# Optimization experiments

Measured on AMD Instinct MI355X. Metric: run time of the kernel, lower is better.

## Reference

```python
import jax, jax.numpy as jnp
import numpy as np

N = 100000   # num_nodes
E = 1600000  # num_edges
H = 128      # hidden_dim
OUT = 1      # output_dim
SLOPE = 0.2  # GATConv leaky_relu negative_slope


def setup_inputs() -> dict:
    key = jax.random.key(0)
    ks = jax.random.split(key, 10)
    s = 1.0 / np.sqrt(H)
    return {
        "h": jnp.arange(N, dtype=jnp.int64 if jax.config.jax_enable_x64 else jnp.int32),
        "edge_index": jax.random.randint(ks[0], (2, E), 0, N),
        "node_type": jax.random.randint(ks[1], (N,), 0, 3),
        "emb": jax.random.normal(ks[2], (N, H), jnp.float32) * s,
        "W1": jax.random.normal(ks[3], (H, H), jnp.float32) * s,
        "a_src1": jax.random.normal(ks[4], (H,), jnp.float32) * s,
        "a_dst1": jax.random.normal(ks[5], (H,), jnp.float32) * s,
        "b1": jnp.zeros((H,), jnp.float32),
        "W2": jax.random.normal(ks[6], (H, OUT), jnp.float32) * s,
        "a_src2": jax.random.normal(ks[7], (OUT,), jnp.float32) * s,
        "a_dst2": jax.random.normal(ks[8], (OUT,), jnp.float32) * s,
        "b2": jnp.zeros((OUT,), jnp.float32),
    }


def gat_layer(x, src, dst, emask, W, a_src, a_dst, b, n_nodes):
    """PyG GATConv (heads=1, add_self_loops=True). Masked edges get -inf logits."""
    xp = x @ W                                  # [N, F]
    e_src = xp @ a_src                          # [N]
    e_dst = xp @ a_dst                          # [N]
    logits = jax.nn.leaky_relu(e_src[src] + e_dst[dst], SLOPE)   # [E]
    logits = jnp.where(emask, logits, -jnp.inf)
    self_logits = jax.nn.leaky_relu(e_src + e_dst, SLOPE)        # [N] self-loops
    # segment softmax over destination nodes (edges + self loop)
    m = jax.ops.segment_max(logits, dst, num_segments=n_nodes)
    m = jnp.maximum(m, self_logits)             # finite: self loop always present
    ew = jnp.exp(logits - m[dst])               # masked edges -> exp(-inf)=0
    sw = jnp.exp(self_logits - m)
    denom = jax.ops.segment_sum(ew, dst, num_segments=n_nodes) + sw
    alpha = ew / denom[dst]                     # [E]
    alpha_self = sw / denom                     # [N]
    out = jax.ops.segment_sum(alpha[:, None] * xp[src], dst, num_segments=n_nodes)
    out = out + alpha_self[:, None] * xp + b
    return out


def reference(h, edge_index, node_type, emb, W1, a_src1, a_dst1, b1, W2, a_src2, a_dst2, b2):
    src, dst = edge_index[0], edge_index[1]
    emask = (node_type[src] == 0) & (node_type[dst] == 0)
    x = emb[h]                                          # embedding lookup [N, H]
    x = gat_layer(x, src, dst, emask, W1, a_src1, a_dst1, b1, emb.shape[0])
    x = jax.nn.relu(x)
    x = gat_layer(x, src, dst, emask, W2, a_src2, a_dst2, b2, emb.shape[0])
    return x
```

## Files before the change

kernel.cpp:

```cpp
#include <hip/hip_runtime.h>

#define N_NODES 100000
#define N_EDGES 1600000
#define HD 128
#define SLOPE 0.2f
#define NBLK 391
#define GB 782
#define EB2 3125
#define CAP 32

typedef __attribute__((ext_vector_type(8))) short bf16x8;
typedef __attribute__((ext_vector_type(4))) float f32x4;

__device__ __forceinline__ unsigned short f2bf(float f) {
    union { float f; unsigned u; } v; v.f = f;
    const unsigned u = v.u + 0x7FFFu + ((v.u >> 16) & 1u);
    return (unsigned short)(u >> 16);
}
__device__ __forceinline__ unsigned pack2(float lo, float hi) {
    return (unsigned)f2bf(lo) | ((unsigned)f2bf(hi) << 16);
}
__device__ __forceinline__ float bf2f(unsigned u16) {
    union { unsigned u; float f; } v; v.u = u16 << 16; return v.f;
}

__global__ __launch_bounds__(256) void k0_zero(
    const int* __restrict__ nt, const float* __restrict__ W1,
    int* __restrict__ deg, unsigned* __restrict__ umask,
    unsigned short* __restrict__ W1bfT)
{
    const int i = blockIdx.x * 256 + threadIdx.x;
    bool act = false;
    if (i < N_NODES) { deg[i] = 0; act = (nt[i] == 0); }
    const unsigned long long bal = __ballot(act);
    const int lane = threadIdx.x & 63;
    if (lane == 0)       umask[i >> 5] = (unsigned)bal;
    else if (lane == 32) umask[i >> 5] = (unsigned)(bal >> 32);
    if (i < HD * HD) {
        const int n = i >> 7, k = i & 127;
        W1bfT[n * HD + k] = f2bf(W1[k * HD + n]);
    }
}

__global__ __launch_bounds__(512, 8) void k1_gemm_edge(
    const int* __restrict__ h,
    const float* __restrict__ emb,
    const unsigned short* __restrict__ W1bfT,
    const float* __restrict__ a_src1,
    const float* __restrict__ a_dst1,
    unsigned short* __restrict__ xp1,
    float* __restrict__ es1,
    float* __restrict__ ed1,
    float* __restrict__ denom1,
    const int* __restrict__ ei,
    const unsigned* __restrict__ umask,
    int* __restrict__ deg,
    int* __restrict__ adj)
{
    __shared__ unsigned short Wlds[HD * HD];
    const int tid = threadIdx.x;

    if (blockIdx.x >= GB) {
        const int e = (blockIdx.x - GB) * 512 + tid;
        const int src = ei[e];
        const int dst = ei[N_EDGES + e];
        const bool active =
            (((umask[src >> 5] >> (src & 31)) & (umask[dst >> 5] >> (dst & 31))) & 1u) != 0u;
        if (active) {
            const int slot = atomicAdd(deg + dst, 1);
            if (slot < CAP) adj[(size_t)dst * CAP + slot] = src;
        }
        return;
    }

    {
        const int n  = tid >> 2;
        const int kq = (tid & 3) * 32;
        const unsigned short* src = W1bfT + n * HD + kq;
        #pragma unroll
        for (int j = 0; j < 4; ++j) {
            const int c = (kq >> 3) + j;
            const int p = c ^ (n & 7);
            *(bf16x8*)(Wlds + n * HD + p * 8) = *(const bf16x8*)(src + j * 8);
        }
    }

    const int w   = tid >> 6;
    const int L   = tid & 63;
    const int lm  = L & 15;
    const int lg  = L >> 4;
    const int wrow0 = blockIdx.x * 128 + w * 16;

    const int arow = wrow0 + lm;
    const int g = (arow < N_NODES) ? arow : (N_NODES - 1);
    const float* xrow = emb + (size_t)h[g] * HD;

    __syncthreads();

    f32x4 acc[8];
    #pragma unroll
    for (int ct = 0; ct < 8; ++ct) acc[ct] = (f32x4)0.f;

    #pragma unroll
    for (int ks = 0; ks < 4; ++ks) {
        const int k0 = ks * 32 + lg * 8;
        const float4 u = *(const float4*)(xrow + k0);
        const float4 v = *(const float4*)(xrow + k0 + 4);
        union { bf16x8 b; unsigned x[4]; } t;
        t.x[0] = pack2(u.x, u.y);
        t.x[1] = pack2(u.z, u.w);
        t.x[2] = pack2(v.x, v.y);
        t.x[3] = pack2(v.z, v.w);
        const bf16x8 af = t.b;

        const int c = k0 >> 3;
        const int p = (c ^ (lm & 7)) * 8;
        #pragma unroll
        for (int ct = 0; ct < 8; ++ct) {
            const bf16x8 bfr = *(const bf16x8*)(Wlds + (ct * 16 + lm) * HD + p);
            acc[ct] = __builtin_amdgcn_mfma_f32_16x16x32_bf16(af, bfr, acc[ct], 0, 0, 0);
        }
    }

    float asv[8], adv[8];
    #pragma unroll
    for (int ct = 0; ct < 8; ++ct) {
        asv[ct] = a_src1[ct * 16 + lm];
        adv[ct] = a_dst1[ct * 16 + lm];
    }

    #pragma unroll
    for (int reg = 0; reg < 4; ++reg) {
        const int row = wrow0 + lg * 4 + reg;
        float s = 0.f, d = 0.f;
        #pragma unroll
        for (int ct = 0; ct < 8; ++ct) {
            s += acc[ct][reg] * asv[ct];
            d += acc[ct][reg] * adv[ct];
        }
        #pragma unroll
        for (int m = 1; m < 16; m <<= 1) {
            s += __shfl_xor(s, m, 64);
            d += __shfl_xor(d, m, 64);
        }
        if (row < N_NODES) {
            unsigned short* dst = xp1 + (size_t)row * HD;
            #pragma unroll
            for (int ct = 0; ct < 8; ++ct)
                dst[ct * 16 + lm] = f2bf(acc[ct][reg]);
            if (lm == 0) {
                const float sum = s + d;
                const float l = sum > 0.f ? sum : SLOPE * sum;
                es1[row] = s;
                ed1[row] = d;
                denom1[row] = __expf(l);
            }
        }
    }
}

__global__ __launch_bounds__(256) void k2_gather(
    const unsigned short* __restrict__ xp1, const float* __restrict__ denom1,
    const float* __restrict__ es1, const float* __restrict__ ed1,
    const int* __restrict__ deg, const int* __restrict__ adj,
    const float* __restrict__ b1, const float* __restrict__ W2,
    float* __restrict__ xp2)
{
    const int wid = threadIdx.x >> 6;
    const int lane = threadIdx.x & 63;
    const int i = blockIdx.x * 4 + wid;
    if (i >= N_NODES) return;

    const int dcount = min(deg[i], CAP);
    const float wself = denom1[i];
    const float edv   = ed1[i];
    const int* arow = adj + (size_t)i * CAP;

    const unsigned pself = ((const unsigned*)(xp1 + (size_t)i * HD))[lane];
    float a0 = wself * bf2f(pself & 0xFFFFu);
    float a1 = wself * bf2f(pself >> 16);
    float denom = wself;

    int sN = 0;
    if (dcount > 0) sN = arow[0];
    for (int j = 0; j < dcount; ++j) {
        const int s = sN;
        if (j + 1 < dcount) sN = arow[j + 1];
        const float lg = es1[s] + edv;
        const float l = lg > 0.f ? lg : SLOPE * lg;
        const float w = __expf(l);
        const unsigned pv = ((const unsigned*)(xp1 + (size_t)s * HD))[lane];
        a0 += w * bf2f(pv & 0xFFFFu);
        a1 += w * bf2f(pv >> 16);
        denom += w;
    }

    const float inv = 1.f / denom;
    const float o0 = fmaxf(a0 * inv + b1[2 * lane],     0.f);
    const float o1 = fmaxf(a1 * inv + b1[2 * lane + 1], 0.f);

    float part = o0 * W2[2 * lane] + o1 * W2[2 * lane + 1];
    #pragma unroll
    for (int off = 32; off > 0; off >>= 1) part += __shfl_down(part, off, 64);
    if (lane == 0) xp2[i] = part;
}

__global__ __launch_bounds__(256) void k3_final(
    const float* __restrict__ xp2, const int* __restrict__ deg,
    const int* __restrict__ adj,
    const float* __restrict__ a_src2, const float* __restrict__ a_dst2,
    const float* __restrict__ b2, float* __restrict__ out)
{
    const int i = blockIdx.x * 256 + threadIdx.x;
    if (i >= N_NODES) return;

    const float as = a_src2[0], ad = a_dst2[0];
    const float xi = xp2[i];
    const float s0 = (as + ad) * xi;
    const float l0 = s0 > 0.f ? s0 : SLOPE * s0;
    const float wself = __expf(l0);

    float denom = wself, num = wself * xi;
    const int dcount = min(deg[i], CAP);
    const int* arow = adj + (size_t)i * CAP;
    for (int j = 0; j < dcount; ++j) {
        const float xsv = xp2[arow[j]];
        const float lg = as * xsv + ad * xi;
        const float ll = lg > 0.f ? lg : SLOPE * lg;
        const float w = __expf(ll);
        denom += w;
        num += w * xsv;
    }
    out[i] = num / denom + b2[0];
}

extern "C" void kernel_launch(void* const* d_in, const int* in_sizes, int n_in,
                              void* d_out, int out_size, void* d_ws, size_t ws_size,
                              hipStream_t stream)
{
    const int* h   = (const int*)d_in[0];
    const int* ei  = (const int*)d_in[1];
    const int* nt  = (const int*)d_in[2];
    const float* emb    = (const float*)d_in[3];
    const float* W1     = (const float*)d_in[4];
    const float* a_src1 = (const float*)d_in[5];
    const float* a_dst1 = (const float*)d_in[6];
    const float* b1     = (const float*)d_in[7];
    const float* W2     = (const float*)d_in[8];
    const float* a_src2 = (const float*)d_in[9];
    const float* a_dst2 = (const float*)d_in[10];
    const float* b2     = (const float*)d_in[11];
    float* out = (float*)d_out;

    char* ws = (char*)d_ws;
    size_t off = 0;
    unsigned short* xp1 = (unsigned short*)(ws + off); off += (size_t)N_NODES * HD * sizeof(unsigned short);
    float* es1    = (float*)(ws + off); off += (size_t)N_NODES * sizeof(float);
    float* ed1    = (float*)(ws + off); off += (size_t)N_NODES * sizeof(float);
    float* denom1 = (float*)(ws + off); off += (size_t)N_NODES * sizeof(float);
    float* xp2    = (float*)(ws + off); off += (size_t)N_NODES * sizeof(float);
    int*   deg    = (int*)(ws + off);   off += (size_t)N_NODES * sizeof(int);
    unsigned* umask = (unsigned*)(ws + off); off += 3200 * sizeof(unsigned);
    unsigned short* W1bfT = (unsigned short*)(ws + off); off += (size_t)HD * HD * sizeof(unsigned short);
    off = (off + 255) & ~(size_t)255;
    int*   adj    = (int*)(ws + off);   off += (size_t)N_NODES * CAP * sizeof(int);

    k0_zero<<<NBLK, 256, 0, stream>>>(nt, W1, deg, umask, W1bfT);
    k1_gemm_edge<<<GB + EB2, 512, 0, stream>>>(
        h, emb, W1bfT, a_src1, a_dst1, xp1, es1, ed1, denom1,
        ei, umask, deg, adj);
    k2_gather<<<(N_NODES + 3) / 4, 256, 0, stream>>>(
        xp1, denom1, es1, ed1, deg, adj, b1, W2, xp2);
    k3_final<<<NBLK, 256, 0, stream>>>(
        xp2, deg, adj, a_src2, a_dst2, b2, out);
}
```

Measured before the change: 181.0 us.

## Persist GEMM/edge blocks, stage xp1 stores via LDS, precompute gather weights per lane

The fused GEMM/edge-binning kernel becomes a persistent grid of PB blocks that loop over the virtual block range. Its bf16 output tile is staged through shared memory so each row goes out as coalesced 16-byte stores instead of scattered 2-byte stores. The layer-1 gather now loads neighbour indices and computes attention weights once per lane, reduces the denominator with shuffles, then broadcasts index and weight while unrolling the feature accumulation by two. The layer-2 loop is also unrolled by two with paired index loads. The trade-offs are an extra LDS round trip plus barriers per tile, and a possible load-balance shift from the persistent loop.

Measured after the change: 218.0 us. 20.4% more time.

```diff
diff --git a/kernel.cpp b/kernel.cpp
--- a/kernel.cpp
+++ b/kernel.cpp
@@ -7,6 +7,7 @@
 #define NBLK 391
 #define GB 782
 #define EB2 3125
+#define PB 1024
 #define CAP 32
 
 typedef __attribute__((ext_vector_type(8))) short bf16x8;
@@ -60,100 +61,113 @@
     __shared__ unsigned short Wlds[HD * HD];
     const int tid = threadIdx.x;
 
-    if (blockIdx.x >= GB) {
-        const int e = (blockIdx.x - GB) * 512 + tid;
-        const int src = ei[e];
-        const int dst = ei[N_EDGES + e];
-        const bool active =
-            (((umask[src >> 5] >> (src & 31)) & (umask[dst >> 5] >> (dst & 31))) & 1u) != 0u;
-        if (active) {
-            const int slot = atomicAdd(deg + dst, 1);
-            if (slot < CAP) adj[(size_t)dst * CAP + slot] = src;
-        }
-        return;
-    }
-
-    {
-        const int n  = tid >> 2;
-        const int kq = (tid & 3) * 32;
-        const unsigned short* src = W1bfT + n * HD + kq;
-        #pragma unroll
-        for (int j = 0; j < 4; ++j) {
-            const int c = (kq >> 3) + j;
-            const int p = c ^ (n & 7);
-            *(bf16x8*)(Wlds + n * HD + p * 8) = *(const bf16x8*)(src + j * 8);
-        }
-    }
-
-    const int w   = tid >> 6;
-    const int L   = tid & 63;
-    const int lm  = L & 15;
-    const int lg  = L >> 4;
-    const int wrow0 = blockIdx.x * 128 + w * 16;
-
-    const int arow = wrow0 + lm;
-    const int g = (arow < N_NODES) ? arow : (N_NODES - 1);
-    const float* xrow = emb + (size_t)h[g] * HD;
-
-    __syncthreads();
-
-    f32x4 acc[8];
-    #pragma unroll
-    for (int ct = 0; ct < 8; ++ct) acc[ct] = (f32x4)0.f;
-
-    #pragma unroll
-    for (int ks = 0; ks < 4; ++ks) {
-        const int k0 = ks * 32 + lg * 8;
-        const float4 u = *(const float4*)(xrow + k0);
-        const float4 v = *(const float4*)(xrow + k0 + 4);
-        union { bf16x8 b; unsigned x[4]; } t;
-        t.x[0] = pack2(u.x, u.y);
-        t.x[1] = pack2(u.z, u.w);
-        t.x[2] = pack2(v.x, v.y);
-        t.x[3] = pack2(v.z, v.w);
-        const bf16x8 af = t.b;
-
-        const int c = k0 >> 3;
-        const int p = (c ^ (lm & 7)) * 8;
+    for (int vb = blockIdx.x; vb < GB + EB2; vb += PB) {
+        if (vb >= GB) {
+            const int e = (vb - GB) * 512 + tid;
+            const int src = ei[e];
+            const int dst = ei[N_EDGES + e];
+            const bool active =
+                (((umask[src >> 5] >> (src & 31)) & (umask[dst >> 5] >> (dst & 31))) & 1u) != 0u;
+            if (active) {
+                const int slot = atomicAdd(deg + dst, 1);
+                if (slot < CAP) adj[(size_t)dst * CAP + slot] = src;
+            }
+            continue;
+        }
+
+        {
+            const int n  = tid >> 2;
+            const int kq = (tid & 3) * 32;
+            const unsigned short* src = W1bfT + n * HD + kq;
+            #pragma unroll
+            for (int j = 0; j < 4; ++j) {
+                const int c = (kq >> 3) + j;
+                const int p = c ^ (n & 7);
+                *(bf16x8*)(Wlds + n * HD + p * 8) = *(const bf16x8*)(src + j * 8);
+            }
+        }
+
+        const int w   = tid >> 6;
+        const int L   = tid & 63;
+        const int lm  = L & 15;
+        const int lg  = L >> 4;
+        const int wrow0 = vb * 128 + w * 16;
+
+        const int arow = wrow0 + lm;
+        const int g = (arow < N_NODES) ? arow : (N_NODES - 1);
+        const float* xrow = emb + (size_t)h[g] * HD;
+
+        __syncthreads();
+
+        f32x4 acc[8];
+        #pragma unroll
+        for (int ct = 0; ct < 8; ++ct) acc[ct] = (f32x4)0.f;
+
+        #pragma unroll
+        for (int ks = 0; ks < 4; ++ks) {
+            const int k0 = ks * 32 + lg * 8;
+            const float4 u = *(const float4*)(xrow + k0);
+            const float4 v = *(const float4*)(xrow + k0 + 4);
+            union { bf16x8 b; unsigned x[4]; } t;
+            t.x[0] = pack2(u.x, u.y);
+            t.x[1] = pack2(u.z, u.w);
+            t.x[2] = pack2(v.x, v.y);
+            t.x[3] = pack2(v.z, v.w);
+            const bf16x8 af = t.b;
+
+            const int c = k0 >> 3;
+            const int p = (c ^ (lm & 7)) * 8;
+            #pragma unroll
+            for (int ct = 0; ct < 8; ++ct) {
+                const bf16x8 bfr = *(const bf16x8*)(Wlds + (ct * 16 + lm) * HD + p);
+                acc[ct] = __builtin_amdgcn_mfma_f32_16x16x32_bf16(af, bfr, acc[ct], 0, 0, 0);
+            }
+        }
+
+        float asv[8], adv[8];
         #pragma unroll
         for (int ct = 0; ct < 8; ++ct) {
-            const bf16x8 bfr = *(const bf16x8*)(Wlds + (ct * 16 + lm) * HD + p);
-            acc[ct] = __builtin_amdgcn_mfma_f32_16x16x32_bf16(af, bfr, acc[ct], 0, 0, 0);
-        }
-    }
-
-    float asv[8], adv[8];
-    #pragma unroll
-    for (int ct = 0; ct < 8; ++ct) {
-        asv[ct] = a_src1[ct * 16 + lm];
-        adv[ct] = a_dst1[ct * 16 + lm];
-    }
-
-    #pragma unroll
-    for (int reg = 0; reg < 4; ++reg) {
-        const int row = wrow0 + lg * 4 + reg;
-        float s = 0.f, d = 0.f;
-        #pragma unroll
-        for (int ct = 0; ct < 8; ++ct) {
-            s += acc[ct][reg] * asv[ct];
-            d += acc[ct][reg] * adv[ct];
-        }
-        #pragma unroll
-        for (int m = 1; m < 16; m <<= 1) {
-            s += __shfl_xor(s, m, 64);
-            d += __shfl_xor(d, m, 64);
-        }
-        if (row < N_NODES) {
-            unsigned short* dst = xp1 + (size_t)row * HD;
-            #pragma unroll
-            for (int ct = 0; ct < 8; ++ct)
-                dst[ct * 16 + lm] = f2bf(acc[ct][reg]);
-            if (lm == 0) {
+            asv[ct] = a_src1[ct * 16 + lm];
+            adv[ct] = a_dst1[ct * 16 + lm];
+        }
+
+        #pragma unroll
+        for (int reg = 0; reg < 4; ++reg) {
+            const int row = wrow0 + lg * 4 + reg;
+            float s = 0.f, d = 0.f;
+            #pragma unroll
+            for (int ct = 0; ct < 8; ++ct) {
+                s += acc[ct][reg] * asv[ct];
+                d += acc[ct][reg] * adv[ct];
+            }
+            #pragma unroll
+            for (int m = 1; m < 16; m <<= 1) {
+                s += __shfl_xor(s, m, 64);
+                d += __shfl_xor(d, m, 64);
+            }
+            if (row < N_NODES && lm == 0) {
                 const float sum = s + d;
                 const float l = sum > 0.f ? sum : SLOPE * sum;
                 es1[row] = s;
                 ed1[row] = d;
                 denom1[row] = __expf(l);
+            }
+        }
+
+        __syncthreads();
+        unsigned short* slice = Wlds + w * 2048;
+        #pragma unroll
+        for (int ct = 0; ct < 8; ++ct)
+            #pragma unroll
+            for (int reg = 0; reg < 4; ++reg)
+                slice[(lg * 4 + reg) * HD + ct * 16 + lm] = f2bf(acc[ct][reg]);
+        #pragma unroll
+        for (int rr = 0; rr < 4; ++rr) {
+            const int rl = rr * 4 + lg;
+            const int row = wrow0 + rl;
+            if (row < N_NODES) {
+                const bf16x8 vdat = *(const bf16x8*)(slice + rl * HD + lm * 8);
+                *(bf16x8*)(xp1 + (size_t)row * HD + lm * 8) = vdat;
             }
         }
     }
@@ -176,26 +190,40 @@
     const float edv   = ed1[i];
     const int* arow = adj + (size_t)i * CAP;
 
+    int nidx = 0; float nw = 0.f;
+    if (lane < dcount) {
+        nidx = arow[lane];
+        const float lgt = es1[nidx] + edv;
+        nw = __expf(lgt > 0.f ? lgt : SLOPE * lgt);
+    }
+    float dsum = nw;
+    #pragma unroll
+    for (int m = 32; m > 0; m >>= 1) dsum += __shfl_xor(dsum, m, 64);
+    const float inv = 1.f / (wself + dsum);
+
     const unsigned pself = ((const unsigned*)(xp1 + (size_t)i * HD))[lane];
     float a0 = wself * bf2f(pself & 0xFFFFu);
     float a1 = wself * bf2f(pself >> 16);
-    float denom = wself;
-
-    int sN = 0;
-    if (dcount > 0) sN = arow[0];
-    for (int j = 0; j < dcount; ++j) {
-        const int s = sN;
-        if (j + 1 < dcount) sN = arow[j + 1];
-        const float lg = es1[s] + edv;
-        const float l = lg > 0.f ? lg : SLOPE * lg;
-        const float w = __expf(l);
-        const unsigned pv = ((const unsigned*)(xp1 + (size_t)s * HD))[lane];
-        a0 += w * bf2f(pv & 0xFFFFu);
-        a1 += w * bf2f(pv >> 16);
-        denom += w;
-    }
-
-    const float inv = 1.f / denom;
+
+    int j = 0;
+    for (; j + 2 <= dcount; j += 2) {
+        const int   s0 = __shfl(nidx, j, 64);
+        const int   s1 = __shfl(nidx, j + 1, 64);
+        const float w0 = __shfl(nw, j, 64);
+        const float w1 = __shfl(nw, j + 1, 64);
+        const unsigned p0 = ((const unsigned*)(xp1 + (size_t)s0 * HD))[lane];
+        const unsigned p1 = ((const unsigned*)(xp1 + (size_t)s1 * HD))[lane];
+        a0 += w0 * bf2f(p0 & 0xFFFFu) + w1 * bf2f(p1 & 0xFFFFu);
+        a1 += w0 * bf2f(p0 >> 16)     + w1 * bf2f(p1 >> 16);
+    }
+    if (j < dcount) {
+        const int   s0 = __shfl(nidx, j, 64);
+        const float w0 = __shfl(nw, j, 64);
+        const unsigned p0 = ((const unsigned*)(xp1 + (size_t)s0 * HD))[lane];
+        a0 += w0 * bf2f(p0 & 0xFFFFu);
+        a1 += w0 * bf2f(p0 >> 16);
+    }
+
     const float o0 = fmaxf(a0 * inv + b1[2 * lane],     0.f);
     const float o1 = fmaxf(a1 * inv + b1[2 * lane + 1], 0.f);
 
@@ -216,6 +244,7 @@
 
     const float as = a_src2[0], ad = a_dst2[0];
     const float xi = xp2[i];
+    const float adxi = ad * xi;
     const float s0 = (as + ad) * xi;
     const float l0 = s0 > 0.f ? s0 : SLOPE * s0;
     const float wself = __expf(l0);
@@ -223,13 +252,25 @@
     float denom = wself, num = wself * xi;
     const int dcount = min(deg[i], CAP);
     const int* arow = adj + (size_t)i * CAP;
-    for (int j = 0; j < dcount; ++j) {
-        const float xsv = xp2[arow[j]];
-        const float lg = as * xsv + ad * xi;
-        const float ll = lg > 0.f ? lg : SLOPE * lg;
-        const float w = __expf(ll);
-        denom += w;
-        num += w * xsv;
+
+    int j = 0;
+    for (; j + 2 <= dcount; j += 2) {
+        const int2 ss = *(const int2*)(arow + j);
+        const float x0 = xp2[ss.x];
+        const float x1 = xp2[ss.y];
+        float l0e = as * x0 + adxi; l0e = l0e > 0.f ? l0e : SLOPE * l0e;
+        float l1e = as * x1 + adxi; l1e = l1e > 0.f ? l1e : SLOPE * l1e;
+        const float w0 = __expf(l0e);
+        const float w1 = __expf(l1e);
+        denom += w0 + w1;
+        num   += w0 * x0 + w1 * x1;
+    }
+    if (j < dcount) {
+        const float x0 = xp2[arow[j]];
+        float l0e = as * x0 + adxi; l0e = l0e > 0.f ? l0e : SLOPE * l0e;
+        const float w0 = __expf(l0e);
+        denom += w0;
+        num   += w0 * x0;
     }
     out[i] = num / denom + b2[0];
 }
@@ -266,7 +307,7 @@
     int*   adj    = (int*)(ws + off);   off += (size_t)N_NODES * CAP * sizeof(int);
 
     k0_zero<<<NBLK, 256, 0, stream>>>(nt, W1, deg, umask, W1bfT);
-    k1_gemm_edge<<<GB + EB2, 512, 0, stream>>>(
+    k1_gemm_edge<<<PB, 512, 0, stream>>>(
         h, emb, W1bfT, a_src1, a_dst1, xp1, es1, ed1, denom1,
         ei, umask, deg, adj);
     k2_gather<<<(N_NODES + 3) / 4, 256, 0, stream>>>(
```
